# Kernel optimization log

Measured on AMD Instinct MI355X. Metric: run time of the kernel, lower is better.

Reference implementation:

```python
import jax, jax.numpy as jnp
import numpy as np

NB, C, N, H, W = 2, 128, 4, 64, 64
K = 9  # 3x3 kernel positions


def _conv(x, w, b, pad):
    y = jax.lax.conv_general_dilated(x, w, (1, 1), ((pad, pad), (pad, pad)),
                                     dimension_numbers=('NCHW', 'OIHW', 'NCHW'))
    return y + b[None, :, None, None]


def _bn(x, g, be, m, v, eps=1e-5):
    scale = g / jnp.sqrt(v + eps)
    return x * scale[None, :, None, None] + (be - m * scale)[None, :, None, None]


def _maxpool(x):
    # MaxPool2d(kernel_size=2, stride=1, padding=1): output H+1, W+1
    return jax.lax.reduce_window(x, -jnp.inf, jax.lax.max, (1, 1, 2, 2), (1, 1, 1, 1),
                                 ((0, 0), (0, 0), (1, 1), (1, 1)))


def _deform_conv(x, offset, mask, w, b):
    # modulated deformable conv v2, kernel 3x3, stride 1, padding 1
    n, c, h, wd = x.shape
    ky = jnp.repeat(jnp.arange(3), 3).astype(x.dtype)  # kernel row offsets
    kx = jnp.tile(jnp.arange(3), 3).astype(x.dtype)    # kernel col offsets
    dy = offset[:, 0::2]  # [n,K,h,w] (torchvision layout: interleaved dy,dx)
    dx = offset[:, 1::2]
    py = jnp.arange(h, dtype=x.dtype)[None, None, :, None] - 1.0 + ky[None, :, None, None] + dy
    px = jnp.arange(wd, dtype=x.dtype)[None, None, None, :] - 1.0 + kx[None, :, None, None] + dx
    y0 = jnp.floor(py)
    x0 = jnp.floor(px)
    wy = py - y0
    wx = px - x0
    xt = jnp.transpose(x, (0, 2, 3, 1))  # [n,h,w,c]
    bidx = jnp.arange(n)[:, None, None, None]

    def gather(yi, xi):
        valid = ((yi >= 0) & (yi < h) & (xi >= 0) & (xi < wd)).astype(x.dtype)
        yc = jnp.clip(yi, 0, h - 1).astype(jnp.int32)
        xc = jnp.clip(xi, 0, wd - 1).astype(jnp.int32)
        return xt[bidx, yc, xc] * valid[..., None]  # [n,K,h,w,c]

    v = (((1 - wy) * (1 - wx))[..., None] * gather(y0, x0)
         + ((1 - wy) * wx)[..., None] * gather(y0, x0 + 1)
         + (wy * (1 - wx))[..., None] * gather(y0 + 1, x0)
         + (wy * wx)[..., None] * gather(y0 + 1, x0 + 1))
    v = v * mask[..., None]  # modulation mask [n,K,h,w]
    out = jnp.einsum('nkhwc,ock->nohw', v, w.reshape(w.shape[0], c, K))
    return out + b[None, :, None, None]


def _forward(x, w1, b1, g1, be1, m1, v1, w_off, b_off, w_mod, b_mod, w_def, b_def,
             g2, be2, m2, v2, w_ds, b_ds, g3, be3, m3, v3):
    for i in range(NB):
        h = jax.nn.relu(_bn(_conv(x, w1[i], b1[i], 1), g1[i], be1[i], m1[i], v1[i]))
        off = _conv(h, w_off[i], b_off[i], 1)
        msk = 2.0 * jax.nn.sigmoid(_conv(h, w_mod[i], b_mod[i], 1))
        d = _bn(_deform_conv(h, off, msk, w_def[i], b_def[i]), g2[i], be2[i], m2[i], v2[i])
        res = _bn(_conv(x, w_ds[i], b_ds[i], 0), g3[i], be3[i], m3[i], v3[i])
        x = _maxpool(jax.nn.relu(d + res))
    return x


def setup_inputs() -> dict:
    key = jax.random.key(0)
    ks = iter(jax.random.split(key, 48))

    def rn(shape, s=0.05):
        return jax.random.normal(next(ks), shape, jnp.float32) * s

    def bnp():
        g = jax.random.uniform(next(ks), (NB, C), jnp.float32) * 0.5 + 0.75
        be = rn((NB, C), 0.1)
        m = rn((NB, C), 0.1)
        v = jax.random.uniform(next(ks), (NB, C), jnp.float32) * 0.5 + 0.75
        return g, be, m, v

    g1, be1, m1, v1 = bnp()
    g2, be2, m2, v2 = bnp()
    g3, be3, m3, v3 = bnp()
    return dict(
        x=jax.random.normal(next(ks), (N, C, H, W), jnp.float32),
        w1=rn((NB, C, C, 3, 3)), b1=rn((NB, C)),
        g1=g1, be1=be1, m1=m1, v1=v1,
        w_off=rn((NB, 2 * K, C, 3, 3), 0.01), b_off=rn((NB, 2 * K), 0.01),
        w_mod=rn((NB, K, C, 3, 3), 0.01), b_mod=rn((NB, K), 0.01),
        w_def=rn((NB, C, C, 3, 3)), b_def=rn((NB, C)),
        g2=g2, be2=be2, m2=m2, v2=v2,
        w_ds=rn((NB, C, C, 1, 1)), b_ds=rn((NB, C)),
        g3=g3, be3=be3, m3=m3, v3=v3,
    )


def reference(x, w1, b1, g1, be1, m1, v1, w_off, b_off, w_mod, b_mod, w_def, b_def,
              g2, be2, m2, v2, w_ds, b_ds, g3, be3, m3, v3):
    return _forward(x, w1, b1, g1, be1, m1, v1, w_off, b_off, w_mod, b_mod, w_def, b_def,
                    g2, be2, m2, v2, w_ds, b_ds, g3, be3, m3, v3)
```

## Files before the change

### kernel.cpp

```cpp
#include <hip/hip_runtime.h>
#include <math.h>

constexpr int NN = 4;
constexpr int CC = 128;

typedef unsigned short u16;
typedef short bfrag __attribute__((ext_vector_type(8)));
typedef float facc  __attribute__((ext_vector_type(4)));

__device__ __forceinline__ float bf2f(u16 v) {
    unsigned u = ((unsigned)v) << 16; float f; __builtin_memcpy(&f, &u, 4); return f;
}
__device__ __forceinline__ u16 f2bf(float f) {
    unsigned u; __builtin_memcpy(&u, &f, 4);
    unsigned r = u + 0x7FFFu + ((u >> 16) & 1u);
    return (u16)(r >> 16);
}

typedef const __attribute__((address_space(1))) unsigned int gu32;
typedef __attribute__((address_space(3))) unsigned int lu32;
__device__ __forceinline__ void gload16(const u16* g, u16* l) {
    __builtin_amdgcn_global_load_lds((gu32*)g, (lu32*)l, 16, 0, 0);
}

template<int WM, int WN, int MR, int NR, int NOB, int EPI>
__global__ __launch_bounds__(512)
void gconv_h(const u16* __restrict__ A, const u16* __restrict__ Wp,
             const float* __restrict__ bias, void* __restrict__ Out,
             int H, int W, int npb)
{
    constexpr int HALOW = 68;
    __shared__ __align__(16) u16 halo[4 * HALOW * 128];

    const int Hp = H + 2, Wq = W + 2, HW = H * W;
    const int tid = threadIdx.x, lane = tid & 63, wv = tid >> 6;
    const int wn = wv % WN, wm = wv / WN;
    const int colc = lane & 15, kg = lane >> 4;
    const int n = blockIdx.x / npb;
    const int pib = (blockIdx.x - n * npb) * 64;
    const int ymin = pib / W;

    {
        const u16* Abase = A + (size_t)n * Hp * Wq * 128;
        for (int c = wv; c < 4 * HALOW / 4; c += 8) {
            int o = c * 512 + lane * 8;
            int r = o / (HALOW * 128);
            int e = o - r * (HALOW * 128);
            int x = e >> 7;
            int g = (e >> 3) & 15;
            int xs = x < Wq ? x : Wq - 1;
            int pr = ymin + r; if (pr > Hp - 1) pr = Hp - 1;
            const u16* src = Abase + ((size_t)pr * Wq + xs) * 128 + (g ^ (x & 7)) * 8;
            gload16(src, &halo[c * 512]);
        }
    }
    __syncthreads();

    int dyr[MR], axr[MR];
#pragma unroll
    for (int r = 0; r < MR; ++r) {
        int m = wm * (MR * 16) + r * 16 + colc;
        int pixl = pib + m; if (pixl > HW - 1) pixl = HW - 1;
        int y = pixl / W;
        dyr[r] = y - ymin; axr[r] = pixl - y * W;
    }

    auto wfrag = [&](int tap, int cc, int q) -> const bfrag* {
        return (const bfrag*)(Wp + (size_t)tap * (NOB * 2048)
                              + ((cc * NOB + wn * NR + q) * 64 + lane) * 8);
    };

    bfrag bc[4][NR];
#pragma unroll
    for (int cc = 0; cc < 4; ++cc)
#pragma unroll
        for (int q = 0; q < NR; ++q) bc[cc][q] = *wfrag(0, cc, q);

    facc acc[MR][NR];
#pragma unroll
    for (int r = 0; r < MR; ++r)
#pragma unroll
        for (int q = 0; q < NR; ++q) acc[r][q] = (facc){0.f, 0.f, 0.f, 0.f};

#pragma unroll 1
    for (int t = 0; t < 9; ++t) {
        int ty = t / 3, tx = t - ty * 3;
        bfrag bn_[4][NR];
        if (t < 8) {
#pragma unroll
            for (int cc = 0; cc < 4; ++cc)
#pragma unroll
                for (int q = 0; q < NR; ++q) bn_[cc][q] = *wfrag(t + 1, cc, q);
        }
#pragma unroll
        for (int cc = 0; cc < 4; ++cc) {
            bfrag a[MR];
#pragma unroll
            for (int r = 0; r < MR; ++r) {
                int xx = axr[r] + tx;
                a[r] = *(const bfrag*)&halo[((dyr[r] + ty) * HALOW + xx) * 128
                                            + ((cc * 4 + kg) ^ (xx & 7)) * 8];
            }
#pragma unroll
            for (int r = 0; r < MR; ++r)
#pragma unroll
                for (int q = 0; q < NR; ++q)
                    acc[r][q] = __builtin_amdgcn_mfma_f32_16x16x32_bf16(a[r], bc[cc][q], acc[r][q], 0, 0, 0);
        }
        if (t < 8) {
#pragma unroll
            for (int cc = 0; cc < 4; ++cc)
#pragma unroll
                for (int q = 0; q < NR; ++q) bc[cc][q] = bn_[cc][q];
        }
    }

#pragma unroll
    for (int r = 0; r < MR; ++r) {
#pragma unroll
        for (int j = 0; j < 4; ++j) {
            int m = wm * (MR * 16) + r * 16 + kg * 4 + j;
            int pixl = pib + m;
            if (pixl >= HW) continue;
#pragma unroll
            for (int q = 0; q < NR; ++q) {
                int oc = wn * (NR * 16) + q * 16 + colc;
                float val = acc[r][q][j] + bias[oc];
                if constexpr (EPI == 0) {
                    val = fmaxf(val, 0.f);
                    int y = pixl / W, x = pixl - y * W;
                    ((u16*)Out)[((size_t)(n * Hp + y + 1) * Wq + x + 1) * 128 + oc] = f2bf(val);
                } else {
                    if (oc >= 18) val = 2.f / (1.f + expf(-val));
                    ((float*)Out)[((size_t)n * HW + pixl) * 32 + oc] = val;
                }
            }
        }
    }
}

__global__ __launch_bounds__(512, 2)
void deform6_k(const u16* __restrict__ Hb, const u16* __restrict__ Xp,
               const float* __restrict__ OM, const u16* __restrict__ Wp,
               const float* __restrict__ biasC, float* __restrict__ T,
               int H, int W, int tw, int th)
{
    __shared__ __align__(16) u16 halo[96 * 16 * 8];
    __shared__ __align__(16) u16 Asall[9 * 32 * 128];
    __shared__ __align__(16) float oml[27 * 32];

    const int Hp = H + 2, Wq = W + 2, HW = H * W;
    const int tid = threadIdx.x, lane = tid & 63, wv = tid >> 6;
    const int wn = wv & 3, wm = wv >> 2;
    const int colc = lane & 15, kg = lane >> 4;
    int bt = blockIdx.x;
    int n = bt / (tw * th); int rt = bt - n * (tw * th);
    int ty0 = (rt / tw) * 4, tx0 = (rt - (rt / tw) * tw) * 8;
    const u16* Hbase = Hb + (size_t)n * Hp * Wq * 128;

#pragma unroll
    for (int c = 0; c < 3; ++c) {
        int g = c * 512 + tid;
        int s = g >> 4, u = g & 15;
        int row = s / 12, col = s - row * 12;
        int gy = min(max(ty0 - 2 + row, 0), H - 1);
        int gx = min(max(tx0 - 2 + col, 0), W - 1);
        int gr = u ^ (s & 15);
        gload16(Hbase + ((size_t)(gy + 1) * Wq + gx + 1) * 128 + gr * 8,
                &halo[(c * 512 + wv * 64) * 8]);
    }
    for (int e = tid; e < 27 * 32; e += 512) {
        int f = e >> 5, p = e & 31;
        int yy = min(ty0 + (p >> 3), H - 1), xx = min(tx0 + (p & 7), W - 1);
        oml[e] = OM[((size_t)n * HW + yy * W + xx) * 32 + f];
    }
    __syncthreads();

    {
        const int g0 = tid & 15, m0 = (tid >> 4) & 31;
        const int cy = min(ty0 + (m0 >> 3), H - 1), cx = min(tx0 + (m0 & 7), W - 1);
        const int dslot = (g0 ^ (m0 & 7)) * 8;
#pragma unroll 1
        for (int t = 0; t < 9; ++t) {
            float dy = oml[(2 * t) * 32 + m0];
            float dx = oml[(2 * t + 1) * 32 + m0];
            float mm = oml[(18 + t) * 32 + m0];
            float pyf = (float)cy - 1.f + (float)(t / 3) + dy;
            float pxf = (float)cx - 1.f + (float)(t % 3) + dx;
            float fy = floorf(pyf), fx = floorf(pxf);
            int y0 = (int)fy, x0 = (int)fx;
            float wy = pyf - fy, wx = pxf - fx;
            bool y0v = (y0 >= 0) && (y0 < H), y1v = (y0 >= -1) && (y0 < H - 1);
            bool x0v = (x0 >= 0) && (x0 < W), x1v = (x0 >= -1) && (x0 < W - 1);
            int yc0 = min(max(y0, 0), H - 1), yc1 = min(max(y0 + 1, 0), H - 1);
            int xc0 = min(max(x0, 0), W - 1), xc1 = min(max(x0 + 1, 0), W - 1);
            float w00 = (1.f - wy) * (1.f - wx) * ((y0v && x0v) ? mm : 0.f);
            float w01 = (1.f - wy) * wx         * ((y0v && x1v) ? mm : 0.f);
            float w10 = wy * (1.f - wx)         * ((y1v && x0v) ? mm : 0.f);
            float w11 = wy * wx                 * ((y1v && x1v) ? mm : 0.f);
            int ry0 = yc0 - ty0 + 2, ry1 = yc1 - ty0 + 2;
            int rx0 = xc0 - tx0 + 2, rx1 = xc1 - tx0 + 2;
            bool allin = (unsigned)ry0 < 8u && (unsigned)ry1 < 8u
                      && (unsigned)rx0 < 12u && (unsigned)rx1 < 12u;
            bfrag c00, c01, c10, c11;
            if (allin) {
                int s00 = ry0 * 12 + rx0, s01 = ry0 * 12 + rx1;
                int s10 = ry1 * 12 + rx0, s11 = ry1 * 12 + rx1;
                c00 = *(const bfrag*)&halo[(s00 * 16 + (g0 ^ (s00 & 15))) * 8];
                c01 = *(const bfrag*)&halo[(s01 * 16 + (g0 ^ (s01 & 15))) * 8];
                c10 = *(const bfrag*)&halo[(s10 * 16 + (g0 ^ (s10 & 15))) * 8];
                c11 = *(const bfrag*)&halo[(s11 * 16 + (g0 ^ (s11 & 15))) * 8];
            } else {
                c00 = *(const bfrag*)(Hbase + ((size_t)(yc0 + 1) * Wq + xc0 + 1) * 128 + g0 * 8);
                c01 = *(const bfrag*)(Hbase + ((size_t)(yc0 + 1) * Wq + xc1 + 1) * 128 + g0 * 8);
                c10 = *(const bfrag*)(Hbase + ((size_t)(yc1 + 1) * Wq + xc0 + 1) * 128 + g0 * 8);
                c11 = *(const bfrag*)(Hbase + ((size_t)(yc1 + 1) * Wq + xc1 + 1) * 128 + g0 * 8);
            }
            bfrag o;
#pragma unroll
            for (int j = 0; j < 8; ++j) {
                float f = w00 * bf2f((u16)c00[j]) + w01 * bf2f((u16)c01[j])
                        + w10 * bf2f((u16)c10[j]) + w11 * bf2f((u16)c11[j]);
                o[j] = (short)f2bf(f);
            }
            *(bfrag*)&Asall[t * 4096 + m0 * 128 + dslot] = o;
        }
    }
    __syncthreads();

    const int m = wm * 16 + colc;
    const int cyp = min(ty0 + (m >> 3), H - 1), cxp = min(tx0 + (m & 7), W - 1);
    const size_t xoff = ((size_t)(n * Hp + cyp + 1) * Wq + cxp + 1) * 128;

    auto wfrag = [&](int tap, int cc, int q) -> const bfrag* {
        return (const bfrag*)(Wp + (size_t)tap * 16384
                              + ((cc * 8 + wn * 2 + q) * 64 + lane) * 8);
    };

    bfrag bc[4][2];
#pragma unroll
    for (int cc = 0; cc < 4; ++cc)
#pragma unroll
        for (int q = 0; q < 2; ++q) bc[cc][q] = *wfrag(0, cc, q);

    facc acc[2];
    acc[0] = (facc){0.f, 0.f, 0.f, 0.f};
    acc[1] = (facc){0.f, 0.f, 0.f, 0.f};

#pragma unroll 1
    for (int t = 0; t < 9; ++t) {
        bfrag bn_[4][2];
#pragma unroll
        for (int cc = 0; cc < 4; ++cc)
#pragma unroll
            for (int q = 0; q < 2; ++q) bn_[cc][q] = *wfrag(t + 1, cc, q);
        const u16* as = &Asall[t * 4096];
#pragma unroll
        for (int cc = 0; cc < 4; ++cc) {
            bfrag a = *(const bfrag*)&as[m * 128 + ((cc * 4 + kg) ^ (m & 7)) * 8];
#pragma unroll
            for (int q = 0; q < 2; ++q)
                acc[q] = __builtin_amdgcn_mfma_f32_16x16x32_bf16(a, bc[cc][q], acc[q], 0, 0, 0);
        }
#pragma unroll
        for (int cc = 0; cc < 4; ++cc)
#pragma unroll
            for (int q = 0; q < 2; ++q) bc[cc][q] = bn_[cc][q];
    }
#pragma unroll
    for (int cc = 0; cc < 4; ++cc) {
        bfrag a = *(const bfrag*)(Xp + xoff + (cc * 4 + kg) * 8);
#pragma unroll
        for (int q = 0; q < 2; ++q)
            acc[q] = __builtin_amdgcn_mfma_f32_16x16x32_bf16(a, bc[cc][q], acc[q], 0, 0, 0);
    }

#pragma unroll
    for (int j = 0; j < 4; ++j) {
        int mo = wm * 16 + kg * 4 + j;
        int y = ty0 + (mo >> 3), x = tx0 + (mo & 7);
        if (y >= H || x >= W) continue;
#pragma unroll
        for (int q = 0; q < 2; ++q) {
            int oc = wn * 32 + q * 16 + colc;
            T[((size_t)n * HW + y * W + x) * 128 + oc] = fmaxf(acc[q][j] + biasC[oc], 0.f);
        }
    }
}

template<int OUTMODE>
__global__ __launch_bounds__(256)
void pool_k(const float* __restrict__ T, void* __restrict__ Out, int H, int W)
{
    const int HW = H * W, Ho = H + 1, Wo = W + 1;
    int tot = NN * Ho * Wo * 16;
    int idx = blockIdx.x * 256 + threadIdx.x;
    if (idx >= tot) return;
    int cg = idx & 15; int t = idx >> 4;
    int ox = t % Wo; t /= Wo; int oy = t % Ho; int n = t / Ho;

    float mx[8];
#pragma unroll
    for (int j = 0; j < 8; ++j) mx[j] = -INFINITY;
#pragma unroll
    for (int d = 0; d < 2; ++d) {
        int iy = oy - 1 + d;
        if (iy < 0 || iy >= H) continue;
#pragma unroll
        for (int e = 0; e < 2; ++e) {
            int ix = ox - 1 + e;
            if (ix < 0 || ix >= W) continue;
            const float* src = T + ((size_t)(n * HW + iy * W + ix)) * 128 + cg * 8;
#pragma unroll
            for (int j = 0; j < 8; ++j) mx[j] = fmaxf(mx[j], src[j]);
        }
    }
    if constexpr (OUTMODE == 0) {
        int Hp2 = Ho + 2, Wp2 = Wo + 2;
        bfrag o;
#pragma unroll
        for (int j = 0; j < 8; ++j) o[j] = (short)f2bf(mx[j]);
        *(bfrag*)((u16*)Out + ((size_t)(n * Hp2 + oy + 1) * Wp2 + (ox + 1)) * 128 + cg * 8) = o;
    } else {
#pragma unroll
        for (int j = 0; j < 8; ++j) {
            int c = cg * 8 + j;
            ((float*)Out)[(((size_t)n * 128 + c) * Ho + oy) * Wo + ox] = mx[j];
        }
    }
}

__global__ __launch_bounds__(256)
void prep_k(u16* __restrict__ Xp0, u16* __restrict__ Xp1,
            u16* __restrict__ Hp0, u16* __restrict__ Hp1)
{
    const int G0 = (NN * 66 * 66 * 128) / 8;
    const int G1 = (NN * 67 * 67 * 128) / 8;
    int idx = blockIdx.x * 256 + threadIdx.x;
    bfrag z = (bfrag){0, 0, 0, 0, 0, 0, 0, 0};
    if (idx < G0) { *(bfrag*)(Xp0 + (size_t)idx * 8) = z; return; }
    idx -= G0;
    if (idx < G1) { *(bfrag*)(Xp1 + (size_t)idx * 8) = z; return; }
    idx -= G1;
    if (idx < G0) { *(bfrag*)(Hp0 + (size_t)idx * 8) = z; return; }
    idx -= G0;
    if (idx < G1) { *(bfrag*)(Hp1 + (size_t)idx * 8) = z; return; }
}

__global__ __launch_bounds__(256)
void x0_to_nhwc(const float* __restrict__ x0, u16* __restrict__ Xp)
{
    int idx = blockIdx.x * 256 + threadIdx.x;
    if (idx >= NN * 64 * 64 * 16) return;
    int cg = idx & 15; int t = idx >> 4;
    int x = t & 63; t >>= 6; int y = t & 63; int n = t >> 6;
    bfrag o;
#pragma unroll
    for (int j = 0; j < 8; ++j) {
        int c = cg * 8 + j;
        o[j] = (short)f2bf(x0[(((size_t)n * 128 + c) * 64 + y) * 64 + x]);
    }
    *(bfrag*)(Xp + ((size_t)(n * 66 + y + 1) * 66 + (x + 1)) * 128 + cg * 8) = o;
}

__global__ __launch_bounds__(256)
void wprep_k(const float* __restrict__ w1, const float* __restrict__ b1,
             const float* __restrict__ g1, const float* __restrict__ be1,
             const float* __restrict__ m1, const float* __restrict__ v1,
             const float* __restrict__ w_off, const float* __restrict__ b_off,
             const float* __restrict__ w_mod, const float* __restrict__ b_mod,
             const float* __restrict__ w_def, const float* __restrict__ b_def,
             const float* __restrict__ g2, const float* __restrict__ be2,
             const float* __restrict__ m2, const float* __restrict__ v2,
             const float* __restrict__ w_ds, const float* __restrict__ b_ds,
             const float* __restrict__ g3, const float* __restrict__ be3,
             const float* __restrict__ m3, const float* __restrict__ v3,
             u16* __restrict__ Wb1p, u16* __restrict__ Wbomp, u16* __restrict__ Wbdp,
             float* __restrict__ bias1f, float* __restrict__ biasOM, float* __restrict__ biasC)
{
    const int C1 = 9 * 4 * 8 * 512;
    const int C2 = 9 * 4 * 2 * 512;
    const int C3 = 10 * 4 * 8 * 512;
    int idx = blockIdx.x * 256 + threadIdx.x;
    if (idx < 2 * C1) {
        int inst = idx / C1, e = idx - inst * C1;
        int j = e & 7, lane = (e >> 3) & 63, rest = e >> 9;
        int ob = rest & 7; rest >>= 3; int cc = rest & 3; int tap = rest >> 2;
        int oc = ob * 16 + (lane & 15), c = cc * 32 + (lane >> 4) * 8 + j;
        float sc = g1[inst * 128 + oc] * rsqrtf(v1[inst * 128 + oc] + 1e-5f);
        Wb1p[idx] = f2bf(sc * w1[(((size_t)inst * 128 + oc) * 128 + c) * 9 + tap]);
        return;
    }
    idx -= 2 * C1;
    if (idx < 2 * C2) {
        int inst = idx / C2, e = idx - inst * C2;
        int j = e & 7, lane = (e >> 3) & 63, rest = e >> 9;
        int ob = rest & 1; rest >>= 1; int cc = rest & 3; int tap = rest >> 2;
        int oc = ob * 16 + (lane & 15), c = cc * 32 + (lane >> 4) * 8 + j;
        float v = 0.f;
        if (oc < 18)      v = w_off[(((size_t)inst * 18 + oc) * 128 + c) * 9 + tap];
        else if (oc < 27) v = w_mod[(((size_t)inst * 9 + (oc - 18)) * 128 + c) * 9 + tap];
        Wbomp[inst * C2 + e] = f2bf(v);
        return;
    }
    idx -= 2 * C2;
    if (idx < 2 * C3) {
        int inst = idx / C3, e = idx - inst * C3;
        int j = e & 7, lane = (e >> 3) & 63, rest = e >> 9;
        int ob = rest & 7; rest >>= 3; int cc = rest & 3; int tap = rest >> 2;
        int oc = ob * 16 + (lane & 15), c = cc * 32 + (lane >> 4) * 8 + j;
        float val;
        if (tap < 9) {
            float sc2 = g2[inst * 128 + oc] * rsqrtf(v2[inst * 128 + oc] + 1e-5f);
            val = sc2 * w_def[(((size_t)inst * 128 + oc) * 128 + c) * 9 + tap];
        } else {
            float sc3 = g3[inst * 128 + oc] * rsqrtf(v3[inst * 128 + oc] + 1e-5f);
            val = sc3 * w_ds[((size_t)inst * 128 + oc) * 128 + c];
        }
        Wbdp[inst * C3 + e] = f2bf(val);
        return;
    }
    idx -= 2 * C3;
    if (idx < 2 * 288) {
        int inst = idx / 288, r = idx - inst * 288;
        if (r < 128) {
            int oc = r, o = inst * 128 + oc;
            float sc = g1[o] * rsqrtf(v1[o] + 1e-5f);
            bias1f[o] = sc * b1[o] + be1[o] - m1[o] * sc;
        } else if (r < 160) {
            int oc = r - 128;
            float v = 0.f;
            if (oc < 18)      v = b_off[inst * 18 + oc];
            else if (oc < 27) v = b_mod[inst * 9 + (oc - 18)];
            biasOM[inst * 32 + oc] = v;
        } else {
            int oc = r - 160, o = inst * 128 + oc;
            float sc2 = g2[o] * rsqrtf(v2[o] + 1e-5f);
            float sc3 = g3[o] * rsqrtf(v3[o] + 1e-5f);
            biasC[o] = sc2 * b_def[o] + (be2[o] - m2[o] * sc2)
                     + sc3 * b_ds[o] + (be3[o] - m3[o] * sc3);
        }
    }
}

extern "C" void kernel_launch(void* const* d_in, const int* in_sizes, int n_in,
                              void* d_out, int out_size, void* d_ws, size_t ws_size,
                              hipStream_t stream)
{
    const float* x0    = (const float*)d_in[0];
    const float* w1    = (const float*)d_in[1];
    const float* b1    = (const float*)d_in[2];
    const float* g1    = (const float*)d_in[3];
    const float* be1   = (const float*)d_in[4];
    const float* m1    = (const float*)d_in[5];
    const float* v1    = (const float*)d_in[6];
    const float* w_off = (const float*)d_in[7];
    const float* b_off = (const float*)d_in[8];
    const float* w_mod = (const float*)d_in[9];
    const float* b_mod = (const float*)d_in[10];
    const float* w_def = (const float*)d_in[11];
    const float* b_def = (const float*)d_in[12];
    const float* g2    = (const float*)d_in[13];
    const float* be2   = (const float*)d_in[14];
    const float* m2    = (const float*)d_in[15];
    const float* v2    = (const float*)d_in[16];
    const float* w_ds  = (const float*)d_in[17];
    const float* b_ds  = (const float*)d_in[18];
    const float* g3    = (const float*)d_in[19];
    const float* be3   = (const float*)d_in[20];
    const float* m3    = (const float*)d_in[21];
    const float* v3    = (const float*)d_in[22];

    const int C1 = 147456, C2 = 36864, C3 = 163840;
    char* wsp = (char*)d_ws;
    auto alloc = [&](size_t bytes) { char* r = wsp; wsp += (bytes + 255) & ~(size_t)255; return r; };
    const size_t szX0 = (size_t)NN * 66 * 66 * 128 * 2;
    const size_t szX1 = (size_t)NN * 67 * 67 * 128 * 2;
    u16*   Xpad0  = (u16*)alloc(szX0);
    u16*   Xpad1  = (u16*)alloc(szX1);
    u16*   Hpad0  = (u16*)alloc(szX0);
    u16*   Hpad1  = (u16*)alloc(szX1);
    float* OFFMSK = (float*)alloc((size_t)16900 * 32 * 4);
    float* T      = (float*)alloc((size_t)16900 * 128 * 4);
    u16*   Wb1p   = (u16*)alloc((size_t)2 * C1 * 2);
    u16*   Wbomp  = (u16*)alloc((size_t)2 * C2 * 2);
    u16*   Wbdp   = (u16*)alloc((size_t)2 * C3 * 2);
    float* bias1f = (float*)alloc(2 * 128 * 4);
    float* biasOM = (float*)alloc(2 * 32 * 4);
    float* biasC  = (float*)alloc(2 * 128 * 4);

    const int G0 = (NN * 66 * 66 * 128) / 8, G1 = (NN * 67 * 67 * 128) / 8;
    int ztot = 2 * G0 + 2 * G1;
    prep_k<<<(ztot + 255) / 256, 256, 0, stream>>>(Xpad0, Xpad1, Hpad0, Hpad1);
    x0_to_nhwc<<<(NN * 64 * 64 * 16 + 255) / 256, 256, 0, stream>>>(x0, Xpad0);
    int ptot = 2 * C1 + 2 * C2 + 2 * C3 + 2 * 288;
    wprep_k<<<(ptot + 255) / 256, 256, 0, stream>>>(
        w1, b1, g1, be1, m1, v1, w_off, b_off, w_mod, b_mod, w_def, b_def,
        g2, be2, m2, v2, w_ds, b_ds, g3, be3, m3, v3,
        Wb1p, Wbomp, Wbdp, bias1f, biasOM, biasC);

    const u16* curX = Xpad0;
    for (int i = 0; i < 2; ++i) {
        int H = 64 + i, W = 64 + i;
        int HW = H * W;
        int npb = (HW + 63) / 64;
        int grid = NN * npb;
        u16* Hpad = (i == 0) ? Hpad0 : Hpad1;

        gconv_h<2, 4, 2, 2, 8, 0><<<grid, 512, 0, stream>>>(
            curX, Wb1p + (size_t)i * C1, bias1f + i * 128, Hpad, H, W, npb);
        gconv_h<4, 2, 1, 1, 2, 1><<<grid, 512, 0, stream>>>(
            Hpad, Wbomp + (size_t)i * C2, biasOM + i * 32, OFFMSK, H, W, npb);
        int tw = (W + 7) / 8, th = (H + 3) / 4;
        deform6_k<<<NN * tw * th, 512, 0, stream>>>(
            Hpad, curX, OFFMSK, Wbdp + (size_t)i * C3, biasC + i * 128, T, H, W, tw, th);
        if (i == 0) {
            pool_k<0><<<(NN * 65 * 65 * 16 + 255) / 256, 256, 0, stream>>>(T, Xpad1, H, W);
        } else {
            pool_k<1><<<(NN * 66 * 66 * 16 + 255) / 256, 256, 0, stream>>>(T, d_out, H, W);
        }
        curX = Xpad1;
    }
}
```

Before: 157.9 us.

## Shrink deform LDS to 3-tap ring, raise occupancy, merge prolog kernels

The deformable conv kernel now samples three taps at a time into a small 3-tap LDS buffer and interleaves sampling with MFMA accumulation, instead of staging all nine taps first. This cuts shared memory use so launch bounds can request 4 blocks per CU. It adds extra barriers per tap group. Separately, the zero-fill, input transpose and weight-prep kernels are merged into one prolog kernel, and the fill now zeroes only the padding border instead of the whole buffers, which removes launches and memory traffic. Interior rows of the Xpad1 and Hpad buffers are assumed to be fully written by later kernels.

```diff
diff --git a/kernel.cpp b/kernel.cpp
--- a/kernel.cpp
+++ b/kernel.cpp
@@ -139,14 +139,14 @@
     }
 }
 
-__global__ __launch_bounds__(512, 2)
-void deform6_k(const u16* __restrict__ Hb, const u16* __restrict__ Xp,
+__global__ __launch_bounds__(512, 4)
+void deform7_k(const u16* __restrict__ Hb, const u16* __restrict__ Xp,
                const float* __restrict__ OM, const u16* __restrict__ Wp,
                const float* __restrict__ biasC, float* __restrict__ T,
                int H, int W, int tw, int th)
 {
     __shared__ __align__(16) u16 halo[96 * 16 * 8];
-    __shared__ __align__(16) u16 Asall[9 * 32 * 128];
+    __shared__ __align__(16) u16 As3[3 * 32 * 128];
     __shared__ __align__(16) float oml[27 * 32];
 
     const int Hp = H + 2, Wq = W + 2, HW = H * W;
@@ -176,57 +176,9 @@
     }
     __syncthreads();
 
-    {
-        const int g0 = tid & 15, m0 = (tid >> 4) & 31;
-        const int cy = min(ty0 + (m0 >> 3), H - 1), cx = min(tx0 + (m0 & 7), W - 1);
-        const int dslot = (g0 ^ (m0 & 7)) * 8;
-#pragma unroll 1
-        for (int t = 0; t < 9; ++t) {
-            float dy = oml[(2 * t) * 32 + m0];
-            float dx = oml[(2 * t + 1) * 32 + m0];
-            float mm = oml[(18 + t) * 32 + m0];
-            float pyf = (float)cy - 1.f + (float)(t / 3) + dy;
-            float pxf = (float)cx - 1.f + (float)(t % 3) + dx;
-            float fy = floorf(pyf), fx = floorf(pxf);
-            int y0 = (int)fy, x0 = (int)fx;
-            float wy = pyf - fy, wx = pxf - fx;
-            bool y0v = (y0 >= 0) && (y0 < H), y1v = (y0 >= -1) && (y0 < H - 1);
-            bool x0v = (x0 >= 0) && (x0 < W), x1v = (x0 >= -1) && (x0 < W - 1);
-            int yc0 = min(max(y0, 0), H - 1), yc1 = min(max(y0 + 1, 0), H - 1);
-            int xc0 = min(max(x0, 0), W - 1), xc1 = min(max(x0 + 1, 0), W - 1);
-            float w00 = (1.f - wy) * (1.f - wx) * ((y0v && x0v) ? mm : 0.f);
-            float w01 = (1.f - wy) * wx         * ((y0v && x1v) ? mm : 0.f);
-            float w10 = wy * (1.f - wx)         * ((y1v && x0v) ? mm : 0.f);
-            float w11 = wy * wx                 * ((y1v && x1v) ? mm : 0.f);
-            int ry0 = yc0 - ty0 + 2, ry1 = yc1 - ty0 + 2;
-            int rx0 = xc0 - tx0 + 2, rx1 = xc1 - tx0 + 2;
-            bool allin = (unsigned)ry0 < 8u && (unsigned)ry1 < 8u
-                      && (unsigned)rx0 < 12u && (unsigned)rx1 < 12u;
-            bfrag c00, c01, c10, c11;
-            if (allin) {
-                int s00 = ry0 * 12 + rx0, s01 = ry0 * 12 + rx1;
-                int s10 = ry1 * 12 + rx0, s11 = ry1 * 12 + rx1;
-                c00 = *(const bfrag*)&halo[(s00 * 16 + (g0 ^ (s00 & 15))) * 8];
-                c01 = *(const bfrag*)&halo[(s01 * 16 + (g0 ^ (s01 & 15))) * 8];
-                c10 = *(const bfrag*)&halo[(s10 * 16 + (g0 ^ (s10 & 15))) * 8];
-                c11 = *(const bfrag*)&halo[(s11 * 16 + (g0 ^ (s11 & 15))) * 8];
-            } else {
-                c00 = *(const bfrag*)(Hbase + ((size_t)(yc0 + 1) * Wq + xc0 + 1) * 128 + g0 * 8);
-                c01 = *(const bfrag*)(Hbase + ((size_t)(yc0 + 1) * Wq + xc1 + 1) * 128 + g0 * 8);
-                c10 = *(const bfrag*)(Hbase + ((size_t)(yc1 + 1) * Wq + xc0 + 1) * 128 + g0 * 8);
-                c11 = *(const bfrag*)(Hbase + ((size_t)(yc1 + 1) * Wq + xc1 + 1) * 128 + g0 * 8);
-            }
-            bfrag o;
-#pragma unroll
-            for (int j = 0; j < 8; ++j) {
-                float f = w00 * bf2f((u16)c00[j]) + w01 * bf2f((u16)c01[j])
-                        + w10 * bf2f((u16)c10[j]) + w11 * bf2f((u16)c11[j]);
-                o[j] = (short)f2bf(f);
-            }
-            *(bfrag*)&Asall[t * 4096 + m0 * 128 + dslot] = o;
-        }
-    }
-    __syncthreads();
+    const int g0 = tid & 15, m0 = (tid >> 4) & 31;
+    const int cy1 = min(ty0 + (m0 >> 3), H - 1), cx1 = min(tx0 + (m0 & 7), W - 1);
+    const int dslot = (g0 ^ (m0 & 7)) * 8;
 
     const int m = wm * 16 + colc;
     const int cyp = min(ty0 + (m >> 3), H - 1), cxp = min(tx0 + (m & 7), W - 1);
@@ -237,6 +189,51 @@
                               + ((cc * 8 + wn * 2 + q) * 64 + lane) * 8);
     };
 
+    auto sample1 = [&](int t, int tb) {
+        float dy = oml[(2 * t) * 32 + m0];
+        float dx = oml[(2 * t + 1) * 32 + m0];
+        float mm = oml[(18 + t) * 32 + m0];
+        float pyf = (float)cy1 - 1.f + (float)(t / 3) + dy;
+        float pxf = (float)cx1 - 1.f + (float)(t % 3) + dx;
+        float fy = floorf(pyf), fx = floorf(pxf);
+        int y0 = (int)fy, x0 = (int)fx;
+        float wy = pyf - fy, wx = pxf - fx;
+        bool y0v = (y0 >= 0) && (y0 < H), y1v = (y0 >= -1) && (y0 < H - 1);
+        bool x0v = (x0 >= 0) && (x0 < W), x1v = (x0 >= -1) && (x0 < W - 1);
+        int yc0 = min(max(y0, 0), H - 1), yc1 = min(max(y0 + 1, 0), H - 1);
+        int xc0 = min(max(x0, 0), W - 1), xc1 = min(max(x0 + 1, 0), W - 1);
+        float w00 = (1.f - wy) * (1.f - wx) * ((y0v && x0v) ? mm : 0.f);
+        float w01 = (1.f - wy) * wx         * ((y0v && x1v) ? mm : 0.f);
+        float w10 = wy * (1.f - wx)         * ((y1v && x0v) ? mm : 0.f);
+        float w11 = wy * wx                 * ((y1v && x1v) ? mm : 0.f);
+        int ry0 = yc0 - ty0 + 2, ry1 = yc1 - ty0 + 2;
+        int rx0 = xc0 - tx0 + 2, rx1 = xc1 - tx0 + 2;
+        bool allin = (unsigned)ry0 < 8u && (unsigned)ry1 < 8u
+                  && (unsigned)rx0 < 12u && (unsigned)rx1 < 12u;
+        bfrag c00, c01, c10, c11;
+        if (allin) {
+            int s00 = ry0 * 12 + rx0, s01 = ry0 * 12 + rx1;
+            int s10 = ry1 * 12 + rx0, s11 = ry1 * 12 + rx1;
+            c00 = *(const bfrag*)&halo[(s00 * 16 + (g0 ^ (s00 & 15))) * 8];
+            c01 = *(const bfrag*)&halo[(s01 * 16 + (g0 ^ (s01 & 15))) * 8];
+            c10 = *(const bfrag*)&halo[(s10 * 16 + (g0 ^ (s10 & 15))) * 8];
+            c11 = *(const bfrag*)&halo[(s11 * 16 + (g0 ^ (s11 & 15))) * 8];
+        } else {
+            c00 = *(const bfrag*)(Hbase + ((size_t)(yc0 + 1) * Wq + xc0 + 1) * 128 + g0 * 8);
+            c01 = *(const bfrag*)(Hbase + ((size_t)(yc0 + 1) * Wq + xc1 + 1) * 128 + g0 * 8);
+            c10 = *(const bfrag*)(Hbase + ((size_t)(yc1 + 1) * Wq + xc0 + 1) * 128 + g0 * 8);
+            c11 = *(const bfrag*)(Hbase + ((size_t)(yc1 + 1) * Wq + xc1 + 1) * 128 + g0 * 8);
+        }
+        bfrag o;
+#pragma unroll
+        for (int j = 0; j < 8; ++j) {
+            float f = w00 * bf2f((u16)c00[j]) + w01 * bf2f((u16)c01[j])
+                    + w10 * bf2f((u16)c10[j]) + w11 * bf2f((u16)c11[j]);
+            o[j] = (short)f2bf(f);
+        }
+        *(bfrag*)&As3[tb * 4096 + m0 * 128 + dslot] = o;
+    };
+
     bfrag bc[4][2];
 #pragma unroll
     for (int cc = 0; cc < 4; ++cc)
@@ -248,25 +245,35 @@
     acc[1] = (facc){0.f, 0.f, 0.f, 0.f};
 
 #pragma unroll 1
-    for (int t = 0; t < 9; ++t) {
-        bfrag bn_[4][2];
-#pragma unroll
-        for (int cc = 0; cc < 4; ++cc)
-#pragma unroll
-            for (int q = 0; q < 2; ++q) bn_[cc][q] = *wfrag(t + 1, cc, q);
-        const u16* as = &Asall[t * 4096];
-#pragma unroll
-        for (int cc = 0; cc < 4; ++cc) {
-            bfrag a = *(const bfrag*)&as[m * 128 + ((cc * 4 + kg) ^ (m & 7)) * 8];
-#pragma unroll
-            for (int q = 0; q < 2; ++q)
-                acc[q] = __builtin_amdgcn_mfma_f32_16x16x32_bf16(a, bc[cc][q], acc[q], 0, 0, 0);
-        }
-#pragma unroll
-        for (int cc = 0; cc < 4; ++cc)
-#pragma unroll
-            for (int q = 0; q < 2; ++q) bc[cc][q] = bn_[cc][q];
-    }
+    for (int tg = 0; tg < 3; ++tg) {
+        sample1(tg * 3 + 0, 0);
+        sample1(tg * 3 + 1, 1);
+        sample1(tg * 3 + 2, 2);
+        __syncthreads();
+#pragma unroll
+        for (int tb = 0; tb < 3; ++tb) {
+            int t = tg * 3 + tb;
+            bfrag bn_[4][2];
+#pragma unroll
+            for (int cc = 0; cc < 4; ++cc)
+#pragma unroll
+                for (int q = 0; q < 2; ++q) bn_[cc][q] = *wfrag(t + 1, cc, q);
+            const u16* as = &As3[tb * 4096];
+#pragma unroll
+            for (int cc = 0; cc < 4; ++cc) {
+                bfrag a = *(const bfrag*)&as[m * 128 + ((cc * 4 + kg) ^ (m & 7)) * 8];
+#pragma unroll
+                for (int q = 0; q < 2; ++q)
+                    acc[q] = __builtin_amdgcn_mfma_f32_16x16x32_bf16(a, bc[cc][q], acc[q], 0, 0, 0);
+            }
+#pragma unroll
+            for (int cc = 0; cc < 4; ++cc)
+#pragma unroll
+                for (int q = 0; q < 2; ++q) bc[cc][q] = bn_[cc][q];
+        }
+        __syncthreads();
+    }
+
 #pragma unroll
     for (int cc = 0; cc < 4; ++cc) {
         bfrag a = *(const bfrag*)(Xp + xoff + (cc * 4 + kg) * 8);
@@ -331,57 +338,72 @@
 }
 
 __global__ __launch_bounds__(256)
-void prep_k(u16* __restrict__ Xp0, u16* __restrict__ Xp1,
-            u16* __restrict__ Hp0, u16* __restrict__ Hp1)
+void prolog_k(const float* __restrict__ x0,
+              u16* __restrict__ Xp0, u16* __restrict__ Xp1,
+              u16* __restrict__ Hp0, u16* __restrict__ Hp1,
+              const float* __restrict__ w1, const float* __restrict__ b1,
+              const float* __restrict__ g1, const float* __restrict__ be1,
+              const float* __restrict__ m1, const float* __restrict__ v1,
+              const float* __restrict__ w_off, const float* __restrict__ b_off,
+              const float* __restrict__ w_mod, const float* __restrict__ b_mod,
+              const float* __restrict__ w_def, const float* __restrict__ b_def,
+              const float* __restrict__ g2, const float* __restrict__ be2,
+              const float* __restrict__ m2, const float* __restrict__ v2,
+              const float* __restrict__ w_ds, const float* __restrict__ b_ds,
+              const float* __restrict__ g3, const float* __restrict__ be3,
+              const float* __restrict__ m3, const float* __restrict__ v3,
+              u16* __restrict__ Wb1p, u16* __restrict__ Wbomp, u16* __restrict__ Wbdp,
+              float* __restrict__ bias1f, float* __restrict__ biasOM, float* __restrict__ biasC)
 {
-    const int G0 = (NN * 66 * 66 * 128) / 8;
-    const int G1 = (NN * 67 * 67 * 128) / 8;
+    const int P0 = 260, P1 = 264;
+    const int B0 = NN * P0 * 16, B1 = NN * P1 * 16;
     int idx = blockIdx.x * 256 + threadIdx.x;
     bfrag z = (bfrag){0, 0, 0, 0, 0, 0, 0, 0};
-    if (idx < G0) { *(bfrag*)(Xp0 + (size_t)idx * 8) = z; return; }
-    idx -= G0;
-    if (idx < G1) { *(bfrag*)(Xp1 + (size_t)idx * 8) = z; return; }
-    idx -= G1;
-    if (idx < G0) { *(bfrag*)(Hp0 + (size_t)idx * 8) = z; return; }
-    idx -= G0;
-    if (idx < G1) { *(bfrag*)(Hp1 + (size_t)idx * 8) = z; return; }
-}
-
-__global__ __launch_bounds__(256)
-void x0_to_nhwc(const float* __restrict__ x0, u16* __restrict__ Xp)
-{
-    int idx = blockIdx.x * 256 + threadIdx.x;
-    if (idx >= NN * 64 * 64 * 16) return;
-    int cg = idx & 15; int t = idx >> 4;
-    int x = t & 63; t >>= 6; int y = t & 63; int n = t >> 6;
-    bfrag o;
-#pragma unroll
-    for (int j = 0; j < 8; ++j) {
-        int c = cg * 8 + j;
-        o[j] = (short)f2bf(x0[(((size_t)n * 128 + c) * 64 + y) * 64 + x]);
-    }
-    *(bfrag*)(Xp + ((size_t)(n * 66 + y + 1) * 66 + (x + 1)) * 128 + cg * 8) = o;
-}
-
-__global__ __launch_bounds__(256)
-void wprep_k(const float* __restrict__ w1, const float* __restrict__ b1,
-             const float* __restrict__ g1, const float* __restrict__ be1,
-             const float* __restrict__ m1, const float* __restrict__ v1,
-             const float* __restrict__ w_off, const float* __restrict__ b_off,
-             const float* __restrict__ w_mod, const float* __restrict__ b_mod,
-             const float* __restrict__ w_def, const float* __restrict__ b_def,
-             const float* __restrict__ g2, const float* __restrict__ be2,
-             const float* __restrict__ m2, const float* __restrict__ v2,
-             const float* __restrict__ w_ds, const float* __restrict__ b_ds,
-             const float* __restrict__ g3, const float* __restrict__ be3,
-             const float* __restrict__ m3, const float* __restrict__ v3,
-             u16* __restrict__ Wb1p, u16* __restrict__ Wbomp, u16* __restrict__ Wbdp,
-             float* __restrict__ bias1f, float* __restrict__ biasOM, float* __restrict__ biasC)
-{
+
+    if (idx < 2 * B0) {
+        u16* buf = idx < B0 ? Xp0 : Hp0;
+        int e = idx < B0 ? idx : idx - B0;
+        int gr = e & 15; int t = e >> 4;
+        int b = t % P0; int n = t / P0;
+        int y, x;
+        if (b < 66)        { y = 0;  x = b; }
+        else if (b < 132)  { y = 65; x = b - 66; }
+        else { int r2 = b - 132; y = 1 + (r2 >> 1); x = (r2 & 1) ? 65 : 0; }
+        *(bfrag*)(buf + ((size_t)(n * 66 + y) * 66 + x) * 128 + gr * 8) = z;
+        return;
+    }
+    idx -= 2 * B0;
+    if (idx < 2 * B1) {
+        u16* buf = idx < B1 ? Xp1 : Hp1;
+        int e = idx < B1 ? idx : idx - B1;
+        int gr = e & 15; int t = e >> 4;
+        int b = t % P1; int n = t / P1;
+        int y, x;
+        if (b < 67)        { y = 0;  x = b; }
+        else if (b < 134)  { y = 66; x = b - 67; }
+        else { int r2 = b - 134; y = 1 + (r2 >> 1); x = (r2 & 1) ? 66 : 0; }
+        *(bfrag*)(buf + ((size_t)(n * 67 + y) * 67 + x) * 128 + gr * 8) = z;
+        return;
+    }
+    idx -= 2 * B1;
+
+    if (idx < NN * 64 * 64 * 16) {
+        int cg = idx & 15; int t = idx >> 4;
+        int x = t & 63; t >>= 6; int y = t & 63; int n = t >> 6;
+        bfrag o;
+#pragma unroll
+        for (int j = 0; j < 8; ++j) {
+            int c = cg * 8 + j;
+            o[j] = (short)f2bf(x0[(((size_t)n * 128 + c) * 64 + y) * 64 + x]);
+        }
+        *(bfrag*)(Xp0 + ((size_t)(n * 66 + y + 1) * 66 + (x + 1)) * 128 + cg * 8) = o;
+        return;
+    }
+    idx -= NN * 64 * 64 * 16;
+
     const int C1 = 9 * 4 * 8 * 512;
     const int C2 = 9 * 4 * 2 * 512;
     const int C3 = 10 * 4 * 8 * 512;
-    int idx = blockIdx.x * 256 + threadIdx.x;
     if (idx < 2 * C1) {
         int inst = idx / C1, e = idx - inst * C1;
         int j = e & 7, lane = (e >> 3) & 63, rest = e >> 9;
@@ -489,12 +511,10 @@
     float* biasOM = (float*)alloc(2 * 32 * 4);
     float* biasC  = (float*)alloc(2 * 128 * 4);
 
-    const int G0 = (NN * 66 * 66 * 128) / 8, G1 = (NN * 67 * 67 * 128) / 8;
-    int ztot = 2 * G0 + 2 * G1;
-    prep_k<<<(ztot + 255) / 256, 256, 0, stream>>>(Xpad0, Xpad1, Hpad0, Hpad1);
-    x0_to_nhwc<<<(NN * 64 * 64 * 16 + 255) / 256, 256, 0, stream>>>(x0, Xpad0);
-    int ptot = 2 * C1 + 2 * C2 + 2 * C3 + 2 * 288;
-    wprep_k<<<(ptot + 255) / 256, 256, 0, stream>>>(
+    const int B0 = NN * 260 * 16, B1 = NN * 264 * 16;
+    int ptot = 2 * B0 + 2 * B1 + NN * 64 * 64 * 16 + 2 * C1 + 2 * C2 + 2 * C3 + 2 * 288;
+    prolog_k<<<(ptot + 255) / 256, 256, 0, stream>>>(
+        x0, Xpad0, Xpad1, Hpad0, Hpad1,
         w1, b1, g1, be1, m1, v1, w_off, b_off, w_mod, b_mod, w_def, b_def,
         g2, be2, m2, v2, w_ds, b_ds, g3, be3, m3, v3,
         Wb1p, Wbomp, Wbdp, bias1f, biasOM, biasC);
@@ -512,7 +532,7 @@
         gconv_h<4, 2, 1, 1, 2, 1><<<grid, 512, 0, stream>>>(
             Hpad, Wbomp + (size_t)i * C2, biasOM + i * 32, OFFMSK, H, W, npb);
         int tw = (W + 7) / 8, th = (H + 3) / 4;
-        deform6_k<<<NN * tw * th, 512, 0, stream>>>(
+        deform7_k<<<NN * tw * th, 512, 0, stream>>>(
             Hpad, curX, OFFMSK, Wbdp + (size_t)i * C3, biasC + i * 128, T, H, W, tw, th);
         if (i == 0) {
             pool_k<0><<<(NN * 65 * 65 * 16 + 255) / 256, 256, 0, stream>>>(T, Xpad1, H, W);
```

New measurement: 136.9 us. 1.15x faster.
